# Performance work log

Measured on AMD Instinct MI355X. Metric: run time of the kernel, lower is better.

Reference implementation:

```python
import jax, jax.numpy as jnp
import numpy as np

B, S, D, H, DH = 2, 1024, 1024, 16, 64
SCALE = 1.0 / np.sqrt(DH)


def setup_inputs() -> dict:
    key = jax.random.key(0)
    ks = jax.random.split(key, 9)
    return {
        "x": jax.random.normal(ks[0], (B, S, D), jnp.float32),
        "qkv_w": jax.random.normal(ks[1], (3 * H * DH, D), jnp.float32) * 0.02,
        "out_w": jax.random.normal(ks[2], (D, H * DH), jnp.float32) * 0.02,
        "bias_p": jax.random.uniform(ks[3], (H, 1, 1), jnp.float32) * 2.0,
        "bias_a": jax.random.uniform(ks[4], (H, 1, 1), jnp.float32),
        "mlp_w1": jax.random.normal(ks[5], (H, 2 * H), jnp.float32) * 0.1,
        "mlp_b1": jnp.zeros((H,), jnp.float32),
        "mlp_w2": jax.random.normal(ks[6], (H, H), jnp.float32) * 0.1,
        "mlp_b2": jnp.zeros((H,), jnp.float32),
    }


def reference(x, qkv_w, out_w, bias_p, bias_a, mlp_w1, mlp_b1, mlp_w2, mlp_b2):
    # qkv projection: torch Linear => x @ W.T
    qkv = (x @ qkv_w.T).reshape(B, S, 3, H, DH)
    q = qkv[:, :, 0].transpose(0, 2, 1, 3)  # [B,H,S,DH]
    k = qkv[:, :, 1].transpose(0, 2, 1, 3)
    v = qkv[:, :, 2].transpose(0, 2, 1, 3)

    scores = jnp.einsum('bhqd,bhkd->bhqk', q, k) * SCALE  # [B,H,S,S]

    # Kerple additive bias: -p * log1p(a * |i-j|), per head
    p = jnp.clip(bias_p, 0.01)
    a = jnp.clip(bias_a, 0.01)
    pos = jnp.arange(S, dtype=jnp.float32)
    dist = jnp.abs(pos[None, :] - pos[:, None])  # [S,S]
    kb = -p * jnp.log1p(a * dist)  # [H,S,S]

    # DAPE refinement MLP over per-(i,j) head features
    z = jnp.concatenate(
        [scores, jnp.broadcast_to(kb[None], (B, H, S, S))], axis=1
    ).transpose(0, 2, 3, 1)  # [B,S,S,2H]
    hdn = jax.nn.gelu(z @ mlp_w1.T + mlp_b1, approximate=False)  # [B,S,S,H]
    refine = (hdn @ mlp_w2.T + mlp_b2).transpose(0, 3, 1, 2)  # [B,H,S,S]

    scores = scores + kb[None] + refine
    attn = jax.nn.softmax(scores, axis=-1)  # dropout is identity in eval

    out = jnp.einsum('bhqk,bhkd->bhqd', attn, v)  # [B,H,S,DH]
    out = out.transpose(0, 2, 1, 3).reshape(B, S, H * DH)
    return out @ out_w.T
```

## Files before the change

kernel.cpp:

```cpp
#include <hip/hip_runtime.h>
#include <math.h>

#define Bsz 2
#define Ssz 1024
#define Dsz 1024
#define Hn 16
#define DHsz 64
#define QKV3 3072
#define SCALE 0.125f

typedef __bf16 bf16;
typedef bf16 bf16x8 __attribute__((ext_vector_type(8)));
typedef bf16 bf16x4 __attribute__((ext_vector_type(4)));
typedef float f32x4 __attribute__((ext_vector_type(4)));

#define MFMA(a, b, c) __builtin_amdgcn_mfma_f32_16x16x32_bf16(a, b, c, 0, 0, 0)
#define LDT 72

#define SCSLAB(b, i, c) \
  ((size_t)(b) * 16777216 + (size_t)(i) * 16384 + (size_t)(c) * 4096)

__global__ void cast_all(const float* __restrict__ x, const float* __restrict__ qw,
                         const float* __restrict__ ow, bf16* __restrict__ xh,
                         bf16* __restrict__ wh, bf16* __restrict__ owh) {
  int idx = (blockIdx.x * 256 + threadIdx.x) * 4;
  const float* src;
  bf16* dst;
  int off = idx;
  if (idx < 2097152) {
    src = x; dst = xh;
  } else if (idx < 2097152 + 3145728) {
    src = qw; dst = wh; off = idx - 2097152;
  } else {
    src = ow; dst = owh; off = idx - (2097152 + 3145728);
  }
  float4 v = *(const float4*)(src + off);
  bf16x4 hv = {(bf16)v.x, (bf16)v.y, (bf16)v.z, (bf16)v.w};
  *(bf16x4*)(dst + off) = hv;
}

__global__ void tk_wfrag(const float* __restrict__ bias_p, const float* __restrict__ bias_a,
                         const float* __restrict__ w1, const float* __restrict__ b1,
                         const float* __restrict__ w2, float2* __restrict__ tk,
                         bf16* __restrict__ wf) {
  if (blockIdx.x == 128) {
    int lane = threadIdx.x;
    if (lane < 64) {
      int l15 = lane & 15, q8 = (lane >> 4) << 3;
      bf16x8 w1d, w2a;
#pragma unroll
      for (int e = 0; e < 8; ++e) {
        int k = q8 + e;
        if (k < 16) {
          w1d[e] = (bf16)w1[l15 * 32 + k];
        } else {
          float w = w1[l15 * 32 + k - 16];
          w1d[e] = (bf16)(w - (float)(bf16)w);
        }
        w2a[e] = (bf16)w2[l15 * 16 + (k & 15)];
      }
      *(bf16x8*)(wf + lane * 8) = w1d;
      *(bf16x8*)(wf + 512 + lane * 8) = w2a;
    }
    return;
  }
  int idx = blockIdx.x * 256 + threadIdx.x;
  int o = idx >> 4, n = idx & 15;
  int d = o - 1024; if (d < 0) d = -d; if (d > 1023) d = 1023;
  float fd = (float)d;
  float t1 = b1[n];
  float t2 = 0.f;
#pragma unroll
  for (int h = 0; h < 16; ++h) {
    float kb = -fmaxf(bias_p[h], 0.01f) * log1pf(fmaxf(bias_a[h], 0.01f) * fd);
    t1 += w1[n * 32 + 16 + h] * kb;
    if (h == n) t2 = kb;
  }
  tk[idx] = make_float2(t1, t2);
}

__global__ __launch_bounds__(256, 3) void k1_qkv(const bf16* __restrict__ A,
                                                 const bf16* __restrict__ B,
                                                 bf16* __restrict__ C) {
  __shared__ __align__(16) bf16 sA[128 * LDT];
  __shared__ __align__(16) bf16 sB[96 * LDT];
  const int tid = threadIdx.x;
  const int lane = tid & 63, wv = tid >> 6;
  const int wr = wv >> 1, wc = wv & 1;
  const int l15 = lane & 15, q8 = (lane >> 4) << 3, q4 = (lane >> 4) << 2;
  const int m0 = blockIdx.y * 128, n0 = blockIdx.x * 96;
  const int r0 = tid >> 3, c8 = (tid & 7) << 3;

  f32x4 acc[4][3];
#pragma unroll
  for (int t = 0; t < 4; ++t)
#pragma unroll
    for (int u = 0; u < 3; ++u)
#pragma unroll
      for (int r = 0; r < 4; ++r) acc[t][u][r] = 0.f;

  bf16x8 rA[4], rB[3];
#define K1_LOAD(kt)                                                         \
  {                                                                         \
    _Pragma("unroll") for (int c = 0; c < 4; ++c)                           \
      rA[c] = *(const bf16x8*)(A + (size_t)(m0 + c * 32 + r0) * Dsz + (kt) + c8);  \
    _Pragma("unroll") for (int c = 0; c < 3; ++c)                           \
      rB[c] = *(const bf16x8*)(B + (size_t)(n0 + c * 32 + r0) * Dsz + (kt) + c8);  \
  }

  K1_LOAD(0)
  for (int kt = 0; kt < Dsz; kt += 64) {
    __syncthreads();
#pragma unroll
    for (int c = 0; c < 4; ++c) *(bf16x8*)&sA[(c * 32 + r0) * LDT + c8] = rA[c];
#pragma unroll
    for (int c = 0; c < 3; ++c) *(bf16x8*)&sB[(c * 32 + r0) * LDT + c8] = rB[c];
    __syncthreads();
    if (kt + 64 < Dsz) K1_LOAD(kt + 64)
#pragma unroll
    for (int ks = 0; ks < 64; ks += 32) {
      bf16x8 fa[4], fb[3];
#pragma unroll
      for (int t = 0; t < 4; ++t)
        fa[t] = *(const bf16x8*)&sA[(wr * 64 + t * 16 + l15) * LDT + ks + q8];
#pragma unroll
      for (int u = 0; u < 3; ++u)
        fb[u] = *(const bf16x8*)&sB[(wc * 48 + u * 16 + l15) * LDT + ks + q8];
#pragma unroll
      for (int t = 0; t < 4; ++t)
#pragma unroll
        for (int u = 0; u < 3; ++u) acc[t][u] = MFMA(fa[t], fb[u], acc[t][u]);
    }
  }
#undef K1_LOAD

#define K1BST 104
  bf16* sBounce = sA;
#pragma unroll
  for (int t = 0; t < 4; ++t) {
    __syncthreads();
#pragma unroll
    for (int u = 0; u < 3; ++u) {
      int col = wc * 48 + u * 16 + l15;
#pragma unroll
      for (int r = 0; r < 4; ++r)
        sBounce[(wr * 16 + q4 + r) * K1BST + col] = (bf16)acc[t][u][r];
    }
    __syncthreads();
    int lr = tid >> 3;
    int grow = m0 + (lr < 16 ? t * 16 + lr : 64 + t * 16 + (lr - 16));
#pragma unroll
    for (int cg = 0; cg < 3; ++cg) {
      int cc = cg * 32 + (tid & 7) * 4;
      bf16x4 vv = *(const bf16x4*)&sBounce[lr * K1BST + cc];
      *(bf16x4*)(C + (size_t)grow * QKV3 + n0 + cc) = vv;
    }
  }
#undef K1BST
}

__global__ void pack_vt(const bf16* __restrict__ qkv, bf16* __restrict__ vt) {
  __shared__ __align__(16) bf16 T[64 * LDT];
  const int tid = threadIdx.x;
  const int bh = blockIdx.y, b = bh >> 4, h = bh & 15;
  const int j0 = blockIdx.x * 64;
#pragma unroll
  for (int c = 0; c < 2; ++c) {
    int lin = c * 256 + tid;
    int jr = lin >> 3, d8 = (lin & 7) << 3;
    bf16x8 v = *(const bf16x8*)(qkv + (size_t)(b * Ssz + j0 + jr) * QKV3 + 2048 + h * DHsz + d8);
#pragma unroll
    for (int e = 0; e < 8; ++e) T[(d8 + e) * LDT + jr] = v[e];
  }
  __syncthreads();
#pragma unroll
  for (int c = 0; c < 2; ++c) {
    int lin = c * 256 + tid;
    int d = lin >> 3, j8 = (lin & 7) << 3;
    bf16x8 o = *(const bf16x8*)&T[d * LDT + j8];
    *(bf16x8*)(vt + ((size_t)(b * Hn + h) * DHsz + d) * Ssz + j0 + j8) = o;
  }
}

__global__ __launch_bounds__(256, 3) void k2_qk(const bf16* __restrict__ qkv,
                                                bf16* __restrict__ scores) {
  __shared__ __align__(16) bf16 sA[128 * LDT], sB[128 * LDT];
  const int tid = threadIdx.x;
  const int lane = tid & 63, wv = tid >> 6;
  const int wr = wv >> 1, wc = wv & 1;
  const int l15 = lane & 15, q8 = (lane >> 4) << 3, q4 = (lane >> 4) << 2;
  const int z = blockIdx.z, b = z >> 4, h = z & 15;
  const int i0 = blockIdx.y * 128, j0 = blockIdx.x * 128;
  const bf16* Ab = qkv + (size_t)b * Ssz * QKV3 + h * DHsz;
  const bf16* Bb = Ab + Ssz;
  const int r0 = tid >> 3, c8 = (tid & 7) << 3;
#pragma unroll
  for (int c = 0; c < 4; ++c) {
    int row = c * 32 + r0;
    *(bf16x8*)&sA[row * LDT + c8] = *(const bf16x8*)(Ab + (size_t)(i0 + row) * QKV3 + c8);
    *(bf16x8*)&sB[row * LDT + c8] = *(const bf16x8*)(Bb + (size_t)(j0 + row) * QKV3 + c8);
  }
  __syncthreads();
  f32x4 acc[4][4];
#pragma unroll
  for (int t = 0; t < 4; ++t)
#pragma unroll
    for (int u = 0; u < 4; ++u)
#pragma unroll
      for (int r = 0; r < 4; ++r) acc[t][u][r] = 0.f;
#pragma unroll
  for (int ks = 0; ks < 64; ks += 32) {
    bf16x8 fa[4], fb[4];
#pragma unroll
    for (int t = 0; t < 4; ++t) fa[t] = *(const bf16x8*)&sA[(wr * 64 + t * 16 + l15) * LDT + ks + q8];
#pragma unroll
    for (int u = 0; u < 4; ++u) fb[u] = *(const bf16x8*)&sB[(wc * 64 + u * 16 + l15) * LDT + ks + q8];
#pragma unroll
    for (int t = 0; t < 4; ++t)
#pragma unroll
      for (int u = 0; u < 4; ++u) acc[t][u] = MFMA(fa[t], fb[u], acc[t][u]);
  }

#define K2BST 136
  bf16* sBounce = sA;
  const int chnk = j0 >> 8, jhalf = j0 & 128;
  bf16* base2 = scores + SCSLAB(b, 0, chnk) + h * 256 + jhalf;
#pragma unroll
  for (int t = 0; t < 4; ++t) {
    __syncthreads();
#pragma unroll
    for (int u = 0; u < 4; ++u) {
      int col = wc * 64 + u * 16 + l15;
#pragma unroll
      for (int r = 0; r < 4; ++r)
        sBounce[(wr * 16 + q4 + r) * K2BST + col] = (bf16)(acc[t][u][r] * SCALE);
    }
    __syncthreads();
#pragma unroll
    for (int hf = 0; hf < 2; ++hf) {
      int lr = hf * 16 + (tid >> 4);
      int cc = (tid & 15) * 8;
      bf16x8 vv = *(const bf16x8*)&sBounce[lr * K2BST + cc];
      int grow = i0 + (lr < 16 ? t * 16 + lr : 64 + t * 16 + (lr - 16));
      *(bf16x8*)(base2 + (size_t)grow * 16384 + cc) = vv;
    }
  }
#undef K2BST
}

__device__ __forceinline__ float gelu_fast(float x) {
  float z = fabsf(x) * 0.70710678118654752f;
  float t = __builtin_amdgcn_rcpf(fmaf(0.47047f, z, 1.0f));
  float poly = t * fmaf(t, fmaf(t, 0.7478556f, -0.0958798f), 0.3480242f);
  float erfa = 1.0f - poly * __expf(-z * z);
  float erfs = copysignf(erfa, x);
  return 0.5f * x * (1.0f + erfs);
}

#define SHS 264

__global__ __launch_bounds__(1024, 8) void dape_softmax(bf16* scores,
                                                        const float2* __restrict__ tk,
                                                        const bf16* __restrict__ wf,
                                                        const float* __restrict__ b2,
                                                        float* __restrict__ sums) {
  const int i = blockIdx.x;
  const int b = blockIdx.y;
  const int tid = threadIdx.x;
  const int w = tid >> 6, lane = tid & 63;
  const int c = w >> 2;
  const int l15 = lane & 15, q = lane >> 4;
  const int q8 = q << 3, q4 = q << 2;

  __shared__ bf16 sH[4][Hn][SHS];
  __shared__ __align__(16) bf16 hdnS[16][16][40];
  __shared__ float sumLDS[16][16];

  const bf16x8 w1d = *(const bf16x8*)(wf + lane * 8);
  const bf16x8 w2a = *(const bf16x8*)(wf + 512 + lane * 8);
  const float bias2 = b2[l15];

  if (lane < 32) {
    int row = lane >> 1, col = 16 + (lane & 1) * 8;
    *(bf16x8*)&hdnS[w][row][col] = (bf16x8){};
  }

  const int jw = (w & 3) * 64;
  bf16* slab = scores + SCSLAB(b, i, c);
#pragma unroll
  for (int t = 0; t < 2; ++t) {
    int h = t * 8 + (lane >> 3);
    int col = jw + (lane & 7) * 8;
    *(bf16x8*)&sH[c][h][col] = *(const bf16x8*)(slab + h * 256 + col);
  }

  const float2* tkp = tk + ((size_t)(c * 256 + jw + q4 - i + 1024) << 4) + l15;
  bf16* prow = slab + l15 * 256 + jw;
  float psum = 0.f;

#pragma unroll
  for (int jt = 0; jt < 4; ++jt) {
    const int j0c = jw + jt * 16;
    bf16x8 a1;
#pragma unroll
    for (int e = 0; e < 8; ++e) a1[e] = sH[c][(q8 + e) & 15][j0c + l15];
    float2 tkv[4];
#pragma unroll
    for (int r = 0; r < 4; ++r) tkv[r] = tkp[jt * 256 + r * 16];
    f32x4 c1 = {tkv[0].x, tkv[1].x, tkv[2].x, tkv[3].x};
    c1 = MFMA(a1, w1d, c1);
#pragma unroll
    for (int r = 0; r < 4; ++r) hdnS[w][q4 + r][l15] = (bf16)gelu_fast(c1[r]);
    bf16x8 a2 = *(const bf16x8*)&hdnS[w][l15][q8];
    f32x4 c2 = {bias2, bias2, bias2, bias2};
    c2 = MFMA(a2, w2a, c2);
    bf16x4 sc4 = *(const bf16x4*)&sH[c][l15][j0c + q4];
    f32x4 pv;
#pragma unroll
    for (int r = 0; r < 4; ++r) {
      float lg = (float)sc4[r] + tkv[r].y + c2[r];
      pv[r] = __expf(lg);
      psum += pv[r];
    }
    bf16x4 p4 = {(bf16)pv[0], (bf16)pv[1], (bf16)pv[2], (bf16)pv[3]};
    *(bf16x4*)(prow + jt * 16 + q4) = p4;
  }

  psum += __shfl_xor(psum, 16, 64);
  psum += __shfl_xor(psum, 32, 64);
  if (lane < 16) sumLDS[w][lane] = psum;
  __syncthreads();
  if (tid < 16) {
    int h = tid;
    float s0 = ((sumLDS[0][h] + sumLDS[1][h]) + sumLDS[2][h]) + sumLDS[3][h];
    float s1 = ((sumLDS[4][h] + sumLDS[5][h]) + sumLDS[6][h]) + sumLDS[7][h];
    float s2 = ((sumLDS[8][h] + sumLDS[9][h]) + sumLDS[10][h]) + sumLDS[11][h];
    float s3 = ((sumLDS[12][h] + sumLDS[13][h]) + sumLDS[14][h]) + sumLDS[15][h];
    sums[(((b << 10) + i) << 4) + h] = ((s0 + s1) + s2) + s3;
  }
}

__global__ __launch_bounds__(256, 6) void k4_av(const bf16* __restrict__ attn,
                                                const bf16* __restrict__ vt,
                                                const float* __restrict__ sums,
                                                bf16* __restrict__ aout) {
  __shared__ __align__(16) bf16 sA[64 * LDT], sB[64 * LDT];
  const int tid = threadIdx.x;
  const int lane = tid & 63, wv = tid >> 6;
  const int wr = wv >> 1, wc = wv & 1;
  const int l15 = lane & 15, q8 = (lane >> 4) << 3, q4 = (lane >> 4) << 2;
  const int i0 = blockIdx.x * 64, h = blockIdx.y, b = blockIdx.z;
  const bf16* Ab = attn + SCSLAB(b, i0, 0) + h * 256;
  const bf16* Bb = vt + (size_t)(b * Hn + h) * DHsz * Ssz;
  const int r0 = tid >> 3, c8 = (tid & 7) << 3;
  f32x4 acc[2][2];
#pragma unroll
  for (int t = 0; t < 2; ++t)
#pragma unroll
    for (int u = 0; u < 2; ++u)
#pragma unroll
      for (int r = 0; r < 4; ++r) acc[t][u][r] = 0.f;
  bf16x8 rA[2], rB[2];
#define K4_LOAD(kt)                                                          \
  {                                                                          \
    _Pragma("unroll") for (int c = 0; c < 2; ++c) {                          \
      int row = c * 32 + r0;                                                 \
      rA[c] = *(const bf16x8*)(Ab + (size_t)row * 16384 +                    \
                               (((kt) >> 8) * 4096) + ((kt) & 255) + c8);    \
      rB[c] = *(const bf16x8*)(Bb + ((size_t)row << 10) + (kt) + c8);        \
    }                                                                        \
  }
  K4_LOAD(0)
  for (int kt = 0; kt < Ssz; kt += 64) {
    __syncthreads();
#pragma unroll
    for (int c = 0; c < 2; ++c) {
      int row = c * 32 + r0;
      *(bf16x8*)&sA[row * LDT + c8] = rA[c];
      *(bf16x8*)&sB[row * LDT + c8] = rB[c];
    }
    __syncthreads();
    if (kt + 64 < Ssz) K4_LOAD(kt + 64)
#pragma unroll
    for (int ks = 0; ks < 64; ks += 32) {
      bf16x8 fa[2], fb[2];
#pragma unroll
      for (int t = 0; t < 2; ++t) fa[t] = *(const bf16x8*)&sA[(wr * 32 + t * 16 + l15) * LDT + ks + q8];
#pragma unroll
      for (int u = 0; u < 2; ++u) fb[u] = *(const bf16x8*)&sB[(wc * 32 + u * 16 + l15) * LDT + ks + q8];
#pragma unroll
      for (int t = 0; t < 2; ++t)
#pragma unroll
        for (int u = 0; u < 2; ++u) acc[t][u] = MFMA(fa[t], fb[u], acc[t][u]);
    }
  }
#undef K4_LOAD

  bf16* sBounce = sA;
  __syncthreads();
#pragma unroll
  for (int t = 0; t < 2; ++t)
#pragma unroll
    for (int r = 0; r < 4; ++r) {
      int lr = wr * 32 + t * 16 + q4 + r;
      int row = i0 + lr;
      float inv = 1.f / sums[(((b << 10) + row) << 4) + h];
#pragma unroll
      for (int u = 0; u < 2; ++u)
        sBounce[lr * LDT + wc * 32 + u * 16 + l15] = (bf16)(acc[t][u][r] * inv);
    }
  __syncthreads();
#pragma unroll
  for (int r2 = 0; r2 < 2; ++r2) {
    int lr = r2 * 32 + (tid >> 3);
    int cc = (tid & 7) * 8;
    bf16x8 vv = *(const bf16x8*)&sBounce[lr * LDT + cc];
    *(bf16x8*)(aout + (size_t)(b * Ssz + i0 + lr) * Dsz + h * DHsz + cc) = vv;
  }
}

__global__ __launch_bounds__(256, 6) void k5_out(const bf16* __restrict__ A,
                                                 const bf16* __restrict__ B,
                                                 float* __restrict__ C) {
  __shared__ __align__(16) bf16 sA[64 * LDT], sB[64 * LDT];
  const int tid = threadIdx.x;
  const int lane = tid & 63, wv = tid >> 6;
  const int wr = wv >> 1, wc = wv & 1;
  const int l15 = lane & 15, q8 = (lane >> 4) << 3, q4 = (lane >> 4) << 2;
  const int m0 = blockIdx.y * 64, n0 = blockIdx.x * 64;
  const int r0 = tid >> 3, c8 = (tid & 7) << 3;
  f32x4 acc[2][2];
#pragma unroll
  for (int t = 0; t < 2; ++t)
#pragma unroll
    for (int u = 0; u < 2; ++u)
#pragma unroll
      for (int r = 0; r < 4; ++r) acc[t][u][r] = 0.f;
  bf16x8 rA[2], rB[2];
#define K5_LOAD(kt)                                                       \
  {                                                                       \
    _Pragma("unroll") for (int c = 0; c < 2; ++c) {                       \
      int row = c * 32 + r0;                                              \
      rA[c] = *(const bf16x8*)(A + (size_t)(m0 + row) * Dsz + (kt) + c8);   \
      rB[c] = *(const bf16x8*)(B + (size_t)(n0 + row) * Dsz + (kt) + c8);   \
    }                                                                     \
  }
  K5_LOAD(0)
  for (int kt = 0; kt < Dsz; kt += 64) {
    __syncthreads();
#pragma unroll
    for (int c = 0; c < 2; ++c) {
      int row = c * 32 + r0;
      *(bf16x8*)&sA[row * LDT + c8] = rA[c];
      *(bf16x8*)&sB[row * LDT + c8] = rB[c];
    }
    __syncthreads();
    if (kt + 64 < Dsz) K5_LOAD(kt + 64)
#pragma unroll
    for (int ks = 0; ks < 64; ks += 32) {
      bf16x8 fa[2], fb[2];
#pragma unroll
      for (int t = 0; t < 2; ++t) fa[t] = *(const bf16x8*)&sA[(wr * 32 + t * 16 + l15) * LDT + ks + q8];
#pragma unroll
      for (int u = 0; u < 2; ++u) fb[u] = *(const bf16x8*)&sB[(wc * 32 + u * 16 + l15) * LDT + ks + q8];
#pragma unroll
      for (int t = 0; t < 2; ++t)
#pragma unroll
        for (int u = 0; u < 2; ++u) acc[t][u] = MFMA(fa[t], fb[u], acc[t][u]);
    }
  }
#pragma unroll
  for (int t = 0; t < 2; ++t)
#pragma unroll
    for (int u = 0; u < 2; ++u) {
      int col = n0 + wc * 32 + u * 16 + l15;
#pragma unroll
      for (int r = 0; r < 4; ++r) {
        int row = m0 + wr * 32 + t * 16 + q4 + r;
        C[(size_t)row * Dsz + col] = acc[t][u][r];
      }
    }
#undef K5_LOAD
}

extern "C" void kernel_launch(void* const* d_in, const int* in_sizes, int n_in,
                              void* d_out, int out_size, void* d_ws, size_t ws_size,
                              hipStream_t stream) {
  const float* x      = (const float*)d_in[0];
  const float* qkv_w  = (const float*)d_in[1];
  const float* out_w  = (const float*)d_in[2];
  const float* bias_p = (const float*)d_in[3];
  const float* bias_a = (const float*)d_in[4];
  const float* w1     = (const float*)d_in[5];
  const float* b1     = (const float*)d_in[6];
  const float* w2     = (const float*)d_in[7];
  const float* b2     = (const float*)d_in[8];
  float* out = (float*)d_out;

  char* ws = (char*)d_ws;
  const size_t MB = 1ull << 20;
  bf16* ow_h   = (bf16*)(ws + 0 * MB);
  bf16* qkv_bf = (bf16*)(ws + 2 * MB);
  bf16* v_t    = (bf16*)(ws + 14 * MB);
  bf16* aout   = (bf16*)(ws + 18 * MB);
  float* sums  = (float*)(ws + 22 * MB + 65536);
  bf16* wf     = (bf16*)(ws + 22 * MB + 589824);
  float2* tk   = (float2*)(ws + 22 * MB + 655360);
  bf16* x_h    = (bf16*)(ws + 23 * MB);
  bf16* w_h    = (bf16*)(ws + 27 * MB);
  bf16* sc_bf  = (bf16*)(ws + 23 * MB);

  cast_all<<<6144, 256, 0, stream>>>(x, qkv_w, out_w, x_h, w_h, ow_h);
  tk_wfrag<<<129, 256, 0, stream>>>(bias_p, bias_a, w1, b1, w2, tk, wf);

  k1_qkv<<<dim3(QKV3 / 96, (Bsz * Ssz) / 128), 256, 0, stream>>>(x_h, w_h, qkv_bf);
  pack_vt<<<dim3(Ssz / 64, Bsz * Hn), 256, 0, stream>>>(qkv_bf, v_t);

  k2_qk<<<dim3(Ssz / 128, Ssz / 128, Bsz * Hn), 256, 0, stream>>>(qkv_bf, sc_bf);
  dape_softmax<<<dim3(Ssz, Bsz), 1024, 0, stream>>>(sc_bf, tk, wf, b2, sums);
  k4_av<<<dim3(Ssz / 64, Hn, Bsz), 256, 0, stream>>>(sc_bf, v_t, sums, aout);

  k5_out<<<dim3(Dsz / 64, (Bsz * Ssz) / 64), 256, 0, stream>>>(aout, ow_h, out);
}
```

Before: 198.1 us.

## Double-buffer QKV GEMM via direct global-to-LDS loads and merge prep kernels

The QKV projection GEMM now stages tiles straight from global memory into LDS with global_load_lds into a double buffer. This replaces the register round-trip and one of the two barriers per k-step, and lets the next tile load overlap the MFMA work. The unpadded LDS layout may add bank conflicts on fragment reads, and the doubled LDS footprint lowers the occupancy target from 3 to 2 blocks. The cast kernel and the bias/weight-fragment kernel are also fused into one launch to save launch overhead.

Result: slower. 207.5 us (+4.8%).

```diff
diff --git a/kernel.cpp b/kernel.cpp
--- a/kernel.cpp
+++ b/kernel.cpp
@@ -20,30 +20,40 @@
 #define SCSLAB(b, i, c) \
   ((size_t)(b) * 16777216 + (size_t)(i) * 16384 + (size_t)(c) * 4096)
 
-__global__ void cast_all(const float* __restrict__ x, const float* __restrict__ qw,
-                         const float* __restrict__ ow, bf16* __restrict__ xh,
-                         bf16* __restrict__ wh, bf16* __restrict__ owh) {
-  int idx = (blockIdx.x * 256 + threadIdx.x) * 4;
-  const float* src;
-  bf16* dst;
-  int off = idx;
-  if (idx < 2097152) {
-    src = x; dst = xh;
-  } else if (idx < 2097152 + 3145728) {
-    src = qw; dst = wh; off = idx - 2097152;
-  } else {
-    src = ow; dst = owh; off = idx - (2097152 + 3145728);
-  }
-  float4 v = *(const float4*)(src + off);
-  bf16x4 hv = {(bf16)v.x, (bf16)v.y, (bf16)v.z, (bf16)v.w};
-  *(bf16x4*)(dst + off) = hv;
-}
-
-__global__ void tk_wfrag(const float* __restrict__ bias_p, const float* __restrict__ bias_a,
-                         const float* __restrict__ w1, const float* __restrict__ b1,
-                         const float* __restrict__ w2, float2* __restrict__ tk,
-                         bf16* __restrict__ wf) {
-  if (blockIdx.x == 128) {
+__device__ __forceinline__ void gstage(const bf16* g, size_t ldg, bf16* ldsbase,
+                                       int lane) {
+  __builtin_amdgcn_global_load_lds(
+      (const __attribute__((address_space(1))) void*)(g + (size_t)(lane >> 3) * ldg +
+                                                      ((lane & 7) << 3)),
+      (__attribute__((address_space(3))) void*)ldsbase, 16, 0, 0);
+}
+
+__global__ void prep(const float* __restrict__ x, const float* __restrict__ qw,
+                     const float* __restrict__ ow, bf16* __restrict__ xh,
+                     bf16* __restrict__ wh, bf16* __restrict__ owh,
+                     const float* __restrict__ bias_p, const float* __restrict__ bias_a,
+                     const float* __restrict__ w1, const float* __restrict__ b1,
+                     const float* __restrict__ w2, float2* __restrict__ tk,
+                     bf16* __restrict__ wf) {
+  const int bid = blockIdx.x;
+  if (bid < 6144) {
+    int idx = (bid * 256 + threadIdx.x) * 4;
+    const float* src;
+    bf16* dst;
+    int off = idx;
+    if (idx < 2097152) {
+      src = x; dst = xh;
+    } else if (idx < 2097152 + 3145728) {
+      src = qw; dst = wh; off = idx - 2097152;
+    } else {
+      src = ow; dst = owh; off = idx - (2097152 + 3145728);
+    }
+    float4 v = *(const float4*)(src + off);
+    bf16x4 hv = {(bf16)v.x, (bf16)v.y, (bf16)v.z, (bf16)v.w};
+    *(bf16x4*)(dst + off) = hv;
+    return;
+  }
+  if (bid == 6272) {
     int lane = threadIdx.x;
     if (lane < 64) {
       int l15 = lane & 15, q8 = (lane >> 4) << 3;
@@ -64,7 +74,7 @@
     }
     return;
   }
-  int idx = blockIdx.x * 256 + threadIdx.x;
+  int idx = (bid - 6144) * 256 + threadIdx.x;
   int o = idx >> 4, n = idx & 15;
   int d = o - 1024; if (d < 0) d = -d; if (d > 1023) d = 1023;
   float fd = (float)d;
@@ -79,17 +89,16 @@
   tk[idx] = make_float2(t1, t2);
 }
 
-__global__ __launch_bounds__(256, 3) void k1_qkv(const bf16* __restrict__ A,
+__global__ __launch_bounds__(256, 2) void k1_qkv(const bf16* __restrict__ A,
                                                  const bf16* __restrict__ B,
                                                  bf16* __restrict__ C) {
-  __shared__ __align__(16) bf16 sA[128 * LDT];
-  __shared__ __align__(16) bf16 sB[96 * LDT];
+  __shared__ __align__(16) bf16 sA[2][128 * 64];
+  __shared__ __align__(16) bf16 sB[2][96 * 64];
   const int tid = threadIdx.x;
   const int lane = tid & 63, wv = tid >> 6;
   const int wr = wv >> 1, wc = wv & 1;
   const int l15 = lane & 15, q8 = (lane >> 4) << 3, q4 = (lane >> 4) << 2;
   const int m0 = blockIdx.y * 128, n0 = blockIdx.x * 96;
-  const int r0 = tid >> 3, c8 = (tid & 7) << 3;
 
   f32x4 acc[4][3];
 #pragma unroll
@@ -99,43 +108,42 @@
 #pragma unroll
       for (int r = 0; r < 4; ++r) acc[t][u][r] = 0.f;
 
-  bf16x8 rA[4], rB[3];
-#define K1_LOAD(kt)                                                         \
+#define K1_STAGE(buf, kt)                                                   \
   {                                                                         \
     _Pragma("unroll") for (int c = 0; c < 4; ++c)                           \
-      rA[c] = *(const bf16x8*)(A + (size_t)(m0 + c * 32 + r0) * Dsz + (kt) + c8);  \
+      gstage(A + (size_t)(m0 + wv * 32 + c * 8) * Dsz + (kt), Dsz,          \
+             &sA[buf][(wv * 32 + c * 8) * 64], lane);                       \
     _Pragma("unroll") for (int c = 0; c < 3; ++c)                           \
-      rB[c] = *(const bf16x8*)(B + (size_t)(n0 + c * 32 + r0) * Dsz + (kt) + c8);  \
-  }
-
-  K1_LOAD(0)
+      gstage(B + (size_t)(n0 + wv * 24 + c * 8) * Dsz + (kt), Dsz,          \
+             &sB[buf][(wv * 24 + c * 8) * 64], lane);                       \
+  }
+
+  K1_STAGE(0, 0)
+  __syncthreads();
+  int cur = 0;
   for (int kt = 0; kt < Dsz; kt += 64) {
-    __syncthreads();
-#pragma unroll
-    for (int c = 0; c < 4; ++c) *(bf16x8*)&sA[(c * 32 + r0) * LDT + c8] = rA[c];
-#pragma unroll
-    for (int c = 0; c < 3; ++c) *(bf16x8*)&sB[(c * 32 + r0) * LDT + c8] = rB[c];
-    __syncthreads();
-    if (kt + 64 < Dsz) K1_LOAD(kt + 64)
+    if (kt + 64 < Dsz) K1_STAGE(cur ^ 1, kt + 64)
 #pragma unroll
     for (int ks = 0; ks < 64; ks += 32) {
       bf16x8 fa[4], fb[3];
 #pragma unroll
       for (int t = 0; t < 4; ++t)
-        fa[t] = *(const bf16x8*)&sA[(wr * 64 + t * 16 + l15) * LDT + ks + q8];
+        fa[t] = *(const bf16x8*)&sA[cur][(wr * 64 + t * 16 + l15) * 64 + ks + q8];
 #pragma unroll
       for (int u = 0; u < 3; ++u)
-        fb[u] = *(const bf16x8*)&sB[(wc * 48 + u * 16 + l15) * LDT + ks + q8];
+        fb[u] = *(const bf16x8*)&sB[cur][(wc * 48 + u * 16 + l15) * 64 + ks + q8];
 #pragma unroll
       for (int t = 0; t < 4; ++t)
 #pragma unroll
         for (int u = 0; u < 3; ++u) acc[t][u] = MFMA(fa[t], fb[u], acc[t][u]);
     }
-  }
-#undef K1_LOAD
+    __syncthreads();
+    cur ^= 1;
+  }
+#undef K1_STAGE
 
 #define K1BST 104
-  bf16* sBounce = sA;
+  bf16* sBounce = &sA[0][0];
 #pragma unroll
   for (int t = 0; t < 4; ++t) {
     __syncthreads();
@@ -510,8 +518,8 @@
   bf16* w_h    = (bf16*)(ws + 27 * MB);
   bf16* sc_bf  = (bf16*)(ws + 23 * MB);
 
-  cast_all<<<6144, 256, 0, stream>>>(x, qkv_w, out_w, x_h, w_h, ow_h);
-  tk_wfrag<<<129, 256, 0, stream>>>(bias_p, bias_a, w1, b1, w2, tk, wf);
+  prep<<<6273, 256, 0, stream>>>(x, qkv_w, out_w, x_h, w_h, ow_h,
+                                 bias_p, bias_a, w1, b1, w2, tk, wf);
 
   k1_qkv<<<dim3(QKV3 / 96, (Bsz * Ssz) / 128), 256, 0, stream>>>(x_h, w_h, qkv_bf);
   pack_vt<<<dim3(Ssz / 64, Bsz * Hn), 256, 0, stream>>>(qkv_bf, v_t);
```
